# Optimization experiments

Measured on AMD Instinct MI355X. Metric: run time of the kernel, lower is better.

## Reference

```python
import jax, jax.numpy as jnp
import numpy as np

MAX_VARS = 10
EMBED_DIM = 128
PATCH = (16, 16)


def setup_inputs() -> dict:
    key = jax.random.key(0)
    k1, k2, k3, k4 = jax.random.split(key, 4)
    x = jax.random.normal(k1, (16, 8, 512, 512), dtype=jnp.float32)
    in_vars = jax.random.randint(k2, (8,), 0, MAX_VARS, dtype=jnp.int64)
    proj_weights = jax.random.normal(k3, (MAX_VARS, EMBED_DIM, 1, PATCH[0], PATCH[1]), dtype=jnp.float32)
    proj_biases = jax.random.normal(k4, (MAX_VARS, EMBED_DIM), dtype=jnp.float32)
    return {"x": x, "in_vars": in_vars, "proj_weights": proj_weights, "proj_biases": proj_biases}


def reference(x, in_vars, proj_weights, proj_biases):
    # x: [B, V, H, W]; proj_weights: [max_vars, E, 1, ph, pw]
    B, V, H, W = x.shape
    E, ph, pw = proj_weights.shape[1], proj_weights.shape[3], proj_weights.shape[4]
    gh, gw = H // ph, W // pw
    w = proj_weights[in_vars, :, 0]       # [V, E, ph, pw] gathered per-variable weights
    b = proj_biases[in_vars]              # [V, E]
    # kernel==stride grouped conv == non-overlapping patchify + per-variable matmul
    xp = x.reshape(B, V, gh, ph, gw, pw)
    out = jnp.einsum('bvhpwq,vepq->bvhwe', xp, w)  # [B, V, gh, gw, E]
    out = out.reshape(B, V, gh * gw, E) + b[None, :, None, :]
    return out  # [B, V, num_patches, E]
```

## Files before the change

kernel.cpp:

```cpp
#include <hip/hip_runtime.h>

#define NB 16
#define NV 8
#define HW 512
#define PH 16
#define GH 32
#define ED 128
#define KD 256
#define MAXV 10

typedef __bf16 bf16x8 __attribute__((ext_vector_type(8)));
typedef float  f32x4  __attribute__((ext_vector_type(4)));

__global__ __launch_bounds__(256) void pack_weights(const float* __restrict__ w,
                                                    __bf16* __restrict__ packed) {
    int tid = blockIdx.x * 256 + threadIdx.x;
    if (tid >= MAXV * ED * KD) return;
    int t   = tid & 31;
    int n   = (tid >> 5) & 127;
    int kb  = (tid >> 12) & 7;
    int var = tid >> 15;
    int k   = kb * 32 + t;
    float f = w[(var * ED + n) * KD + k];
    packed[tid] = (__bf16)f;
}

__global__ __launch_bounds__(256, 4) void patch_embed(
    const float* __restrict__ x,
    const int*   __restrict__ in_vars,
    const __bf16* __restrict__ wpacked,
    const float* __restrict__ bias,
    float* __restrict__ out)
{
    const int bx  = blockIdx.x;
    const int h   = bx & 31;
    const int v   = (bx >> 5) & 7;
    const int b   = bx >> 8;
    const int tid = threadIdx.x;

    const int wave = tid >> 6;
    const int lane = tid & 63;
    const int lo   = lane & 15;
    const int quad = lane >> 4;
    const int nwave = wave * 32;

    const int var = in_vars[v];

    const float* xb = x + (((size_t)(b * NV + v)) * HW + (size_t)h * PH) * HW;
    const __bf16* wbase = wpacked + (size_t)var * (ED * KD);

    bf16x8 bF[8][2];
    #pragma unroll
    for (int kb = 0; kb < 8; ++kb)
        #pragma unroll
        for (int j = 0; j < 2; ++j)
            bF[kb][j] = *(const bf16x8*)&wbase[kb * 4096 + (nwave + j * 16 + lo) * 32 + quad * 8];

    f32x4 acc[2][2];
    #pragma unroll
    for (int i = 0; i < 2; ++i)
        #pragma unroll
        for (int j = 0; j < 2; ++j)
            acc[i][j] = (f32x4){0.f, 0.f, 0.f, 0.f};

    const float* abase = xb + (size_t)(quad >> 1) * HW + lo * PH + (quad & 1) * 8;

    #pragma unroll
    for (int kb = 0; kb < 8; ++kb) {
        bf16x8 aF[2];
        #pragma unroll
        for (int i = 0; i < 2; ++i) {
            const float* pA = abase + (size_t)(2 * kb) * HW + i * 256;
            float4 f0 = *(const float4*)pA;
            float4 f1 = *(const float4*)(pA + 4);
            bf16x8 t;
            t[0] = (__bf16)f0.x; t[1] = (__bf16)f0.y; t[2] = (__bf16)f0.z; t[3] = (__bf16)f0.w;
            t[4] = (__bf16)f1.x; t[5] = (__bf16)f1.y; t[6] = (__bf16)f1.z; t[7] = (__bf16)f1.w;
            aF[i] = t;
        }
        #pragma unroll
        for (int i = 0; i < 2; ++i)
            #pragma unroll
            for (int j = 0; j < 2; ++j)
                acc[i][j] = __builtin_amdgcn_mfma_f32_16x16x32_bf16(aF[i], bF[kb][j], acc[i][j], 0, 0, 0);
    }

    float bv[2];
    #pragma unroll
    for (int j = 0; j < 2; ++j)
        bv[j] = bias[var * ED + nwave + j * 16 + lo];

    const size_t outbase = ((size_t)(b * NV + v)) * (GH * GH) + (size_t)h * GH;
    #pragma unroll
    for (int i = 0; i < 2; ++i) {
        #pragma unroll
        for (int r = 0; r < 4; ++r) {
            int m = i * 16 + quad * 4 + r;
            #pragma unroll
            for (int j = 0; j < 2; ++j) {
                int e = nwave + j * 16 + lo;
                out[(outbase + m) * ED + e] = acc[i][j][r] + bv[j];
            }
        }
    }
}

extern "C" void kernel_launch(void* const* d_in, const int* in_sizes, int n_in,
                              void* d_out, int out_size, void* d_ws, size_t ws_size,
                              hipStream_t stream) {
    const float* x       = (const float*)d_in[0];
    const int*   in_vars = (const int*)d_in[1];
    const float* w       = (const float*)d_in[2];
    const float* bias    = (const float*)d_in[3];
    float*       out     = (float*)d_out;
    __bf16*      wpacked = (__bf16*)d_ws;

    hipLaunchKernelGGL(pack_weights, dim3((MAXV * ED * KD + 255) / 256), dim3(256), 0, stream,
                       w, wpacked);
    hipLaunchKernelGGL(patch_embed, dim3(NB * NV * GH), dim3(256), 0, stream,
                       x, in_vars, wpacked, bias, out);
}
```

Baseline: 238.3 us.

## Give each wave a full strip and stream A through LDS via async DMA

Each wave now handles one whole patch row (all 128 embedding columns) instead of four waves splitting the columns. The input strip is prefetched into LDS with global_load_lds in a 4-deep ring, and B fragments are streamed in a 3-deep register ring, with explicit vmcnt waits. This removes redundant A loads across waves and overlaps memory with MFMA, at the cost of more registers, lower occupancy (launch bounds 2) and 64KB of LDS per block.

```diff
diff --git a/kernel.cpp b/kernel.cpp
--- a/kernel.cpp
+++ b/kernel.cpp
@@ -12,6 +12,10 @@
 typedef __bf16 bf16x8 __attribute__((ext_vector_type(8)));
 typedef float  f32x4  __attribute__((ext_vector_type(4)));
 
+template<int N> __device__ __forceinline__ void waitvm() {
+    __builtin_amdgcn_s_waitcnt(0x0F70 | (N & 0xF) | ((N >> 4) << 14));
+}
+
 __global__ __launch_bounds__(256) void pack_weights(const float* __restrict__ w,
                                                     __bf16* __restrict__ packed) {
     int tid = blockIdx.x * 256 + threadIdx.x;
@@ -25,70 +29,96 @@
     packed[tid] = (__bf16)f;
 }
 
-__global__ __launch_bounds__(256, 4) void patch_embed(
+__global__ __launch_bounds__(256, 2) void patch_embed(
     const float* __restrict__ x,
     const int*   __restrict__ in_vars,
     const __bf16* __restrict__ wpacked,
     const float* __restrict__ bias,
     float* __restrict__ out)
 {
-    const int bx  = blockIdx.x;
-    const int h   = bx & 31;
-    const int v   = (bx >> 5) & 7;
-    const int b   = bx >> 8;
-    const int tid = threadIdx.x;
+    __shared__ float As[4 * 1024 * 4];
 
-    const int wave = tid >> 6;
+    const int tid  = threadIdx.x;
+    const int wv   = tid >> 6;
     const int lane = tid & 63;
     const int lo   = lane & 15;
     const int quad = lane >> 4;
-    const int nwave = wave * 32;
+    const int qh   = quad >> 1;
+    const int qlo  = quad & 1;
+
+    const int sid = blockIdx.x * 4 + wv;
+    const int h   = sid & 31;
+    const int v   = (sid >> 5) & 7;
+    const int b   = sid >> 8;
 
     const int var = in_vars[v];
 
-    const float* xb = x + (((size_t)(b * NV + v)) * HW + (size_t)h * PH) * HW;
+    const char* xstrip = (const char*)(x + (((size_t)(b * NV + v)) * HW + (size_t)h * PH) * HW);
     const __bf16* wbase = wpacked + (size_t)var * (ED * KD);
 
-    bf16x8 bF[8][2];
-    #pragma unroll
-    for (int kb = 0; kb < 8; ++kb)
-        #pragma unroll
-        for (int j = 0; j < 2; ++j)
-            bF[kb][j] = *(const bf16x8*)&wbase[kb * 4096 + (nwave + j * 16 + lo) * 32 + quad * 8];
+#define DMA_STAGE(T) { \
+        const char* gsrc = xstrip + (T) * 4096 + lane * 16; \
+        char* lbase = (char*)As + wv * 16384 + ((T) & 3) * 4096; \
+        _Pragma("unroll") for (int c = 0; c < 4; ++c) \
+            __builtin_amdgcn_global_load_lds( \
+                (const __attribute__((address_space(1))) void*)(gsrc + c * 1024), \
+                (__attribute__((address_space(3))) void*)(lbase + c * 1024), 16, 0, 0); }
 
-    f32x4 acc[2][2];
+#define BLOAD(T) { \
+        _Pragma("unroll") for (int j = 0; j < 8; ++j) \
+            bF[(T) % 3][j] = *(const bf16x8*)&wbase[(T) * 4096 + (j * 16 + lo) * 32 + quad * 8]; }
+
+    bf16x8 bF[3][8];
+    f32x4  acc[2][8];
     #pragma unroll
     for (int i = 0; i < 2; ++i)
         #pragma unroll
-        for (int j = 0; j < 2; ++j)
+        for (int j = 0; j < 8; ++j)
             acc[i][j] = (f32x4){0.f, 0.f, 0.f, 0.f};
 
-    const float* abase = xb + (size_t)(quad >> 1) * HW + lo * PH + (quad & 1) * 8;
+    DMA_STAGE(0); DMA_STAGE(1); DMA_STAGE(2); DMA_STAGE(3);
+    asm volatile("" ::: "memory");
+    BLOAD(0); BLOAD(1);
+    asm volatile("" ::: "memory");
 
+#define A_ITER(KB, NW) { \
+        waitvm<NW>(); \
+        asm volatile("" ::: "memory"); \
+        const float* st = As + wv * 4096 + ((KB) & 3) * 1024; \
+        bf16x8 aF[2]; \
+        _Pragma("unroll") for (int i = 0; i < 2; ++i) { \
+            int fo = qh * 512 + (i * 16 + lo) * 16 + qlo * 8; \
+            f32x4 r0 = *(const f32x4*)&st[fo]; \
+            f32x4 r1 = *(const f32x4*)&st[fo + 4]; \
+            bf16x8 t; \
+            t[0] = (__bf16)r0.x; t[1] = (__bf16)r0.y; t[2] = (__bf16)r0.z; t[3] = (__bf16)r0.w; \
+            t[4] = (__bf16)r1.x; t[5] = (__bf16)r1.y; t[6] = (__bf16)r1.z; t[7] = (__bf16)r1.w; \
+            aF[i] = t; } \
+        _Pragma("unroll") for (int i = 0; i < 2; ++i) \
+            _Pragma("unroll") for (int j = 0; j < 8; ++j) \
+                acc[i][j] = __builtin_amdgcn_mfma_f32_16x16x32_bf16(aF[i], bF[(KB) % 3][j], acc[i][j], 0, 0, 0); \
+        asm volatile("" ::: "memory"); \
+        if ((KB) + 2 < 8) BLOAD((KB) + 2); \
+        if ((KB) + 4 < 8) DMA_STAGE((KB) + 4); \
+        asm volatile("" ::: "memory"); }
+
+    A_ITER(0, 8)
+    A_ITER(1, 12)
+    A_ITER(2, 16)
+    A_ITER(3, 16)
+    A_ITER(4, 16)
+    A_ITER(5, 12)
+    A_ITER(6, 8)
+    A_ITER(7, 0)
+
+#undef A_ITER
+#undef BLOAD
+#undef DMA_STAGE
+
+    float bv_[8];
     #pragma unroll
-    for (int kb = 0; kb < 8; ++kb) {
-        bf16x8 aF[2];
-        #pragma unroll
-        for (int i = 0; i < 2; ++i) {
-            const float* pA = abase + (size_t)(2 * kb) * HW + i * 256;
-            float4 f0 = *(const float4*)pA;
-            float4 f1 = *(const float4*)(pA + 4);
-            bf16x8 t;
-            t[0] = (__bf16)f0.x; t[1] = (__bf16)f0.y; t[2] = (__bf16)f0.z; t[3] = (__bf16)f0.w;
-            t[4] = (__bf16)f1.x; t[5] = (__bf16)f1.y; t[6] = (__bf16)f1.z; t[7] = (__bf16)f1.w;
-            aF[i] = t;
-        }
-        #pragma unroll
-        for (int i = 0; i < 2; ++i)
-            #pragma unroll
-            for (int j = 0; j < 2; ++j)
-                acc[i][j] = __builtin_amdgcn_mfma_f32_16x16x32_bf16(aF[i], bF[kb][j], acc[i][j], 0, 0, 0);
-    }
-
-    float bv[2];
-    #pragma unroll
-    for (int j = 0; j < 2; ++j)
-        bv[j] = bias[var * ED + nwave + j * 16 + lo];
+    for (int j = 0; j < 8; ++j)
+        bv_[j] = bias[var * ED + j * 16 + lo];
 
     const size_t outbase = ((size_t)(b * NV + v)) * (GH * GH) + (size_t)h * GH;
     #pragma unroll
@@ -97,9 +127,8 @@
         for (int r = 0; r < 4; ++r) {
             int m = i * 16 + quad * 4 + r;
             #pragma unroll
-            for (int j = 0; j < 2; ++j) {
-                int e = nwave + j * 16 + lo;
-                out[(outbase + m) * ED + e] = acc[i][j][r] + bv[j];
+            for (int j = 0; j < 8; ++j) {
+                out[(outbase + m) * ED + j * 16 + lo] = acc[i][j][r] + bv_[j];
             }
         }
     }
@@ -117,6 +146,6 @@
 
     hipLaunchKernelGGL(pack_weights, dim3((MAXV * ED * KD + 255) / 256), dim3(256), 0, stream,
                        w, wpacked);
-    hipLaunchKernelGGL(patch_embed, dim3(NB * NV * GH), dim3(256), 0, stream,
+    hipLaunchKernelGGL(patch_embed, dim3(NB * NV * GH / 4), dim3(256), 0, stream,
                        x, in_vars, wpacked, bias, out);
 }
```

Measured after the change: 219.6 us. 7.9% less time.

## Give each wave a full patch row and loop over all embedding slices

Applied to the files above, without the earlier changes.

Each wave now owns one (b,v,h) patch row and computes all 128 output channels across four 32-channel passes. Previously the block's four waves split the channels and each loaded the same input. Each wave loads its x data once up front into registers, converts it to bf16, and reuses it for every channel slice. This cuts the redundant input reads by a factor of four and launches a quarter as many blocks. In exchange register pressure rises, so occupancy is lowered to 2 blocks per CU, and the weight fragments are reloaded for each channel slice.

```diff
diff --git a/kernel.cpp b/kernel.cpp
--- a/kernel.cpp
+++ b/kernel.cpp
@@ -21,87 +21,110 @@
     int kb  = (tid >> 12) & 7;
     int var = tid >> 15;
     int k   = kb * 32 + t;
-    float f = w[(var * ED + n) * KD + k];
-    packed[tid] = (__bf16)f;
+    packed[tid] = (__bf16)w[(var * ED + n) * KD + k];
 }
 
-__global__ __launch_bounds__(256, 4) void patch_embed(
+__global__ __launch_bounds__(256, 2) void patch_embed(
     const float* __restrict__ x,
     const int*   __restrict__ in_vars,
     const __bf16* __restrict__ wpacked,
     const float* __restrict__ bias,
     float* __restrict__ out)
 {
-    const int bx  = blockIdx.x;
-    const int h   = bx & 31;
-    const int v   = (bx >> 5) & 7;
-    const int b   = bx >> 8;
-    const int tid = threadIdx.x;
-
-    const int wave = tid >> 6;
+    const int tid  = threadIdx.x;
+    const int wv   = tid >> 6;
     const int lane = tid & 63;
     const int lo   = lane & 15;
     const int quad = lane >> 4;
-    const int nwave = wave * 32;
+    const int qh   = quad >> 1;
+    const int qlo  = quad & 1;
+
+    const int sid = blockIdx.x * 4 + wv;
+    const int h   = sid & 31;
+    const int v   = (sid >> 5) & 7;
+    const int b   = sid >> 8;
 
     const int var = in_vars[v];
 
-    const float* xb = x + (((size_t)(b * NV + v)) * HW + (size_t)h * PH) * HW;
+    const float*  xb    = x + (((size_t)(b * NV + v)) * HW + (size_t)h * PH) * HW;
     const __bf16* wbase = wpacked + (size_t)var * (ED * KD);
+
+    float4 a0[8][2], a1[8][2];
+    const float* abase = xb + qh * HW + lo * PH + qlo * 8;
+    #pragma unroll
+    for (int kb = 0; kb < 8; ++kb)
+        #pragma unroll
+        for (int i = 0; i < 2; ++i) {
+            const float* p = abase + (size_t)(2 * kb) * HW + i * 256;
+            a0[kb][i] = *(const float4*)p;
+            a1[kb][i] = *(const float4*)(p + 4);
+        }
 
     bf16x8 bF[8][2];
     #pragma unroll
     for (int kb = 0; kb < 8; ++kb)
         #pragma unroll
         for (int j = 0; j < 2; ++j)
-            bF[kb][j] = *(const bf16x8*)&wbase[kb * 4096 + (nwave + j * 16 + lo) * 32 + quad * 8];
+            bF[kb][j] = *(const bf16x8*)&wbase[kb * 4096 + (j * 16 + lo) * 32 + quad * 8];
 
-    f32x4 acc[2][2];
+    float bv[4][2];
     #pragma unroll
-    for (int i = 0; i < 2; ++i)
+    for (int ph = 0; ph < 4; ++ph)
         #pragma unroll
         for (int j = 0; j < 2; ++j)
-            acc[i][j] = (f32x4){0.f, 0.f, 0.f, 0.f};
+            bv[ph][j] = bias[var * ED + ph * 32 + j * 16 + lo];
 
-    const float* abase = xb + (size_t)(quad >> 1) * HW + lo * PH + (quad & 1) * 8;
+    asm volatile("" ::: "memory");
+
+    bf16x8 aF[8][2];
+    #pragma unroll
+    for (int kb = 0; kb < 8; ++kb)
+        #pragma unroll
+        for (int i = 0; i < 2; ++i) {
+            bf16x8 t;
+            t[0] = (__bf16)a0[kb][i].x; t[1] = (__bf16)a0[kb][i].y;
+            t[2] = (__bf16)a0[kb][i].z; t[3] = (__bf16)a0[kb][i].w;
+            t[4] = (__bf16)a1[kb][i].x; t[5] = (__bf16)a1[kb][i].y;
+            t[6] = (__bf16)a1[kb][i].z; t[7] = (__bf16)a1[kb][i].w;
+            aF[kb][i] = t;
+        }
+
+    const size_t outbase = ((size_t)(b * NV + v)) * (GH * GH) + (size_t)h * GH;
 
     #pragma unroll
-    for (int kb = 0; kb < 8; ++kb) {
-        bf16x8 aF[2];
-        #pragma unroll
-        for (int i = 0; i < 2; ++i) {
-            const float* pA = abase + (size_t)(2 * kb) * HW + i * 256;
-            float4 f0 = *(const float4*)pA;
-            float4 f1 = *(const float4*)(pA + 4);
-            bf16x8 t;
-            t[0] = (__bf16)f0.x; t[1] = (__bf16)f0.y; t[2] = (__bf16)f0.z; t[3] = (__bf16)f0.w;
-            t[4] = (__bf16)f1.x; t[5] = (__bf16)f1.y; t[6] = (__bf16)f1.z; t[7] = (__bf16)f1.w;
-            aF[i] = t;
+    for (int ph = 0; ph < 4; ++ph) {
+        if (ph > 0) {
+            #pragma unroll
+            for (int kb = 0; kb < 8; ++kb)
+                #pragma unroll
+                for (int j = 0; j < 2; ++j)
+                    bF[kb][j] = *(const bf16x8*)&wbase[kb * 4096 + (ph * 32 + j * 16 + lo) * 32 + quad * 8];
         }
+
+        f32x4 acc[2][2];
         #pragma unroll
         for (int i = 0; i < 2; ++i)
             #pragma unroll
             for (int j = 0; j < 2; ++j)
-                acc[i][j] = __builtin_amdgcn_mfma_f32_16x16x32_bf16(aF[i], bF[kb][j], acc[i][j], 0, 0, 0);
-    }
+                acc[i][j] = (f32x4){0.f, 0.f, 0.f, 0.f};
 
-    float bv[2];
-    #pragma unroll
-    for (int j = 0; j < 2; ++j)
-        bv[j] = bias[var * ED + nwave + j * 16 + lo];
+        #pragma unroll
+        for (int kb = 0; kb < 8; ++kb)
+            #pragma unroll
+            for (int i = 0; i < 2; ++i)
+                #pragma unroll
+                for (int j = 0; j < 2; ++j)
+                    acc[i][j] = __builtin_amdgcn_mfma_f32_16x16x32_bf16(aF[kb][i], bF[kb][j], acc[i][j], 0, 0, 0);
 
-    const size_t outbase = ((size_t)(b * NV + v)) * (GH * GH) + (size_t)h * GH;
-    #pragma unroll
-    for (int i = 0; i < 2; ++i) {
         #pragma unroll
-        for (int r = 0; r < 4; ++r) {
-            int m = i * 16 + quad * 4 + r;
+        for (int i = 0; i < 2; ++i)
             #pragma unroll
-            for (int j = 0; j < 2; ++j) {
-                int e = nwave + j * 16 + lo;
-                out[(outbase + m) * ED + e] = acc[i][j][r] + bv[j];
+            for (int r = 0; r < 4; ++r) {
+                int m = i * 16 + quad * 4 + r;
+                #pragma unroll
+                for (int j = 0; j < 2; ++j)
+                    out[(outbase + m) * ED + ph * 32 + j * 16 + lo] = acc[i][j][r] + bv[ph][j];
             }
-        }
     }
 }
 
@@ -117,6 +140,6 @@
 
     hipLaunchKernelGGL(pack_weights, dim3((MAXV * ED * KD + 255) / 256), dim3(256), 0, stream,
                        w, wpacked);
-    hipLaunchKernelGGL(patch_embed, dim3(NB * NV * GH), dim3(256), 0, stream,
+    hipLaunchKernelGGL(patch_embed, dim3(NB * NV * GH / 4), dim3(256), 0, stream,
                        x, in_vars, wpacked, bias, out);
 }
```

Result: faster. 223.6 us (-6.2%).
